# Kernel tuning notes

Measured on AMD Instinct MI355X. Metric: run time of the kernel, lower is better.

## Reference

```python
import jax, jax.numpy as jnp
import numpy as np

H, W, D, C = 32, 16, 16, 4
NUM_ITERS = 2
THETA_GAMMA = 3.0   # spatial (position-only) kernel bandwidth
THETA_ALPHA = 8.0   # bilateral position bandwidth
THETA_BETA = 0.5    # bilateral color bandwidth


def _attn(feats, q):
    # Gaussian-kernel attention: softmax_j(-0.5 * ||f_i - f_j||^2) @ q
    # feats: [N, F], q: [N, C] -> [N, C]
    sq = jnp.sum(feats * feats, axis=-1)
    logits = feats @ feats.T - 0.5 * (sq[:, None] + sq[None, :])  # [N, N]
    return jax.nn.softmax(logits, axis=-1) @ q


def setup_inputs() -> dict:
    key = jax.random.key(0)
    k1, k2 = jax.random.split(key)
    unaries = jax.random.normal(k1, (1, H, W, D, C), dtype=jnp.float32)
    rgb = jax.random.normal(k2, (1, H, W, D, 3), dtype=jnp.float32)
    eye = jnp.eye(C, dtype=jnp.float32)
    return {
        "unaries": unaries,
        "rgb": rgb,
        "spatial_ker_weights": eye,          # _diagonal_initializer
        "bilateral_ker_weights": eye,        # _diagonal_initializer
        "compatibility_matrix": -eye,        # _potts_model_initializer
    }


def reference(unaries, rgb, spatial_ker_weights, bilateral_ker_weights, compatibility_matrix):
    N = H * W * D
    # positions start at 1 as in tf.range(1, h+1)
    grids = jnp.meshgrid(jnp.arange(1, H + 1), jnp.arange(1, W + 1), jnp.arange(1, D + 1), indexing='ij')
    pos = jnp.stack(grids, axis=-1).astype(jnp.float32).reshape(N, 3)
    rgb_flat = rgb.reshape(N, 3)
    spatial_feats = pos / THETA_GAMMA                                             # [N, 3]
    bilateral_feats = jnp.concatenate([pos / THETA_ALPHA, rgb_flat / THETA_BETA], axis=-1)  # [N, 6]

    u = unaries.reshape(N, C)
    q = u
    for _ in range(NUM_ITERS):
        sm = jax.nn.softmax(q, axis=-1)                         # [N, C]
        spatial_out = _attn(spatial_feats, sm)                  # [N, C]
        bilateral_out = _attn(bilateral_feats, sm)              # [N, C]
        # message_passing = SK @ spatial + BK @ bilateral (class-space matmul)
        message = spatial_out @ spatial_ker_weights.T + bilateral_out @ bilateral_ker_weights.T
        pairwise = message @ compatibility_matrix.T             # [N, C]
        q = u + pairwise
    return q.reshape(unaries.shape)
```

## Files before the change

### kernel.cpp

```cpp
#include <hip/hip_runtime.h>


#define HH 32
#define WW 16
#define DDD 16
#define NN (HH * WW * DDD)
#define KS 128
#define JC (NN / KS)
#define GB 2048
#define L2E 1.4426950408889634f
#define C18 (L2E / 18.0f)
#define SQL2E 1.2011224087864498f
#define SB (SQL2E / 8.0f)
#define SC (SQL2E / 0.5f)

#if __has_builtin(__builtin_amdgcn_exp2f)
#define EXP2(x) __builtin_amdgcn_exp2f(x)
#else
#define EXP2(x) exp2f(x)
#endif

__global__ __launch_bounds__(256, 8) void fused_bilat_conv(
    const float* __restrict__ qin,
    const float* __restrict__ rgb,
    float* __restrict__ part,
    float* __restrict__ tmp)
{
    __shared__ float lds[2048];
    int tid = threadIdx.x;

    if (blockIdx.x < GB) {
        int ib = blockIdx.x >> 7;
        int kc = blockIdx.x & (KS - 1);
        int i0 = ib * 512 + tid;
        int i1 = i0 + 256;
        int j0 = kc * JC;

        float fw = (float)(((tid >> 4) & 15) + 1) * SB;
        float fd = (float)((tid & 15) + 1) * SB;
        int hb = ib * 2;
        float fh = (float)(hb + 1) * SB;
        float c00 = rgb[3 * i0 + 0] * SC;
        float c01 = rgb[3 * i0 + 1] * SC;
        float c02 = rgb[3 * i0 + 2] * SC;
        float c10 = rgb[3 * i1 + 0] * SC;
        float c11 = rgb[3 * i1 + 1] * SC;
        float c12 = rgb[3 * i1 + 2] * SC;
        float fh1 = fh + SB;
        float nn0 = -0.5f * (fh * fh + fw * fw + fd * fd +
                             c00 * c00 + c01 * c01 + c02 * c02);
        float nn1 = -0.5f * (fh1 * fh1 + fw * fw + fd * fd +
                             c10 * c10 + c11 * c11 + c12 * c12);
        float dn = nn1 - nn0;
        float dc0 = c10 - c00, dc1 = c11 - c01, dc2 = c12 - c02;

        float (*recs)[12] = (float(*)[12])lds;
        if (tid < JC) {
            int j = j0 + tid;
            int jh = j >> 8, jr = j & 255;
            float gh = (float)(jh + 1) * SB;
            float gw = (float)((jr >> 4) + 1) * SB;
            float gd = (float)((jr & 15) + 1) * SB;
            float b0 = rgb[3 * j + 0] * SC;
            float b1 = rgb[3 * j + 1] * SC;
            float b2 = rgb[3 * j + 2] * SC;
            float nj = -0.5f * (gh * gh + gw * gw + gd * gd +
                                b0 * b0 + b1 * b1 + b2 * b2);
            float4 q = *((const float4*)(qin + 4 * j));
            float m = fmaxf(fmaxf(q.x, q.y), fmaxf(q.z, q.w));
            float e0 = EXP2((q.x - m) * L2E), e1 = EXP2((q.y - m) * L2E);
            float e2 = EXP2((q.z - m) * L2E), e3 = EXP2((q.w - m) * L2E);
            float rs = 1.0f / (e0 + e1 + e2 + e3);
            *((float4*)&recs[tid][0]) = make_float4(gh, gw, gd, b0);
            *((float4*)&recs[tid][4]) = make_float4(b1, b2, nj, 0.0f);
            *((float4*)&recs[tid][8]) = make_float4(e0 * rs, e1 * rs, e2 * rs, e3 * rs);
        }
        __syncthreads();

        float a0 = 0, a1 = 0, a2 = 0, a3 = 0;
        float b0a = 0, b1a = 0, b2a = 0, b3a = 0;

        #pragma unroll 4
        for (int jj = 0; jj < JC; ++jj) {
            const float4 r0 = *((const float4*)&recs[jj][0]);
            const float4 r1 = *((const float4*)&recs[jj][4]);
            const float4 s  = *((const float4*)&recs[jj][8]);
            float g0 = nn0 + r1.z;
            g0 = fmaf(fh,  r0.x, g0);
            g0 = fmaf(fw,  r0.y, g0);
            g0 = fmaf(fd,  r0.z, g0);
            g0 = fmaf(c00, r0.w, g0);
            g0 = fmaf(c01, r1.x, g0);
            g0 = fmaf(c02, r1.y, g0);
            float g1 = g0 + dn;
            g1 = fmaf(SB,  r0.x, g1);
            g1 = fmaf(dc0, r0.w, g1);
            g1 = fmaf(dc1, r1.x, g1);
            g1 = fmaf(dc2, r1.y, g1);
            float w0 = EXP2(g0);
            float w1 = EXP2(g1);
            a0  = fmaf(w0, s.x, a0);  a1  = fmaf(w0, s.y, a1);
            a2  = fmaf(w0, s.z, a2);  a3  = fmaf(w0, s.w, a3);
            b0a = fmaf(w1, s.x, b0a); b1a = fmaf(w1, s.y, b1a);
            b2a = fmaf(w1, s.z, b2a); b3a = fmaf(w1, s.w, b3a);
        }

        float* p = part + (size_t)kc * (NN * 4);
        *((float4*)(p + (size_t)i0 * 4)) = make_float4(a0, a1, a2, a3);
        *((float4*)(p + (size_t)i1 * 4)) = make_float4(b0a, b1a, b2a, b3a);
    } else {
        int h = blockIdx.x - GB;
        int s = tid;
        int i = h * 256 + s;

        float4 q = *((const float4*)(qin + 4 * i));
        float m = fmaxf(fmaxf(q.x, q.y), fmaxf(q.z, q.w));
        float e0 = EXP2((q.x - m) * L2E), e1 = EXP2((q.y - m) * L2E);
        float e2 = EXP2((q.z - m) * L2E), e3 = EXP2((q.w - m) * L2E);
        float rs = 1.0f / (e0 + e1 + e2 + e3);

        float* A = lds;
        float* B = lds + 1024;
        *((float4*)(A + 4 * s)) = make_float4(e0 * rs, e1 * rs, e2 * rs, e3 * rs);
        __syncthreads();

        int w = s >> 4, d = s & 15;
        float t0 = 0, t1 = 0, t2 = 0, t3 = 0;
        #pragma unroll
        for (int dp = 0; dp < DDD; ++dp) {
            float dd = (float)(d - dp);
            float k = EXP2(-dd * dd * C18);
            const float4 v = *((const float4*)(A + 4 * (w * 16 + dp)));
            t0 = fmaf(k, v.x, t0); t1 = fmaf(k, v.y, t1);
            t2 = fmaf(k, v.z, t2); t3 = fmaf(k, v.w, t3);
        }
        *((float4*)(B + 4 * s)) = make_float4(t0, t1, t2, t3);
        __syncthreads();

        float u0 = 0, u1 = 0, u2 = 0, u3 = 0;
        #pragma unroll
        for (int wp = 0; wp < WW; ++wp) {
            float dw = (float)(w - wp);
            float k = EXP2(-dw * dw * C18);
            const float4 v = *((const float4*)(B + 4 * (wp * 16 + d)));
            u0 = fmaf(k, v.x, u0); u1 = fmaf(k, v.y, u1);
            u2 = fmaf(k, v.z, u2); u3 = fmaf(k, v.w, u3);
        }
        *((float4*)(tmp + 4 * i)) = make_float4(u0, u1, u2, u3);
    }
}

__global__ __launch_bounds__(256) void reduce_finish(
    const float* __restrict__ part,
    const float* __restrict__ tmp,
    const float* __restrict__ u,
    const float* __restrict__ sk, const float* __restrict__ bk,
    const float* __restrict__ cm,
    float* __restrict__ qout)
{
    int tid = threadIdx.x;
    int q = tid >> 6;
    int lane = tid & 63;
    int idx = blockIdx.x * 64 + lane;

    float bl = 0.0f;
    #pragma unroll
    for (int k = 0; k < KS / 4; ++k)
        bl += part[(size_t)(q * (KS / 4) + k) * (NN * 4) + idx];

    int i = idx >> 2;
    int h = i >> 8;
    int scid = idx & 1023;
    float sp = 0.0f;
    #pragma unroll
    for (int k = 0; k < 8; ++k) {
        int hp = q * 8 + k;
        float dh = (float)(h - hp);
        float kk = EXP2(-dh * dh * C18);
        sp = fmaf(kk, tmp[hp * 1024 + scid], sp);
    }

    __shared__ float Lb[4][64];
    __shared__ float Ls[4][64];
    Lb[q][lane] = bl;
    Ls[q][lane] = sp;
    __syncthreads();

    if (tid < 16) {
        float b4[4], s4[4];
        #pragma unroll
        for (int c = 0; c < 4; ++c) {
            int l = tid * 4 + c;
            b4[c] = Lb[0][l] + Lb[1][l] + Lb[2][l] + Lb[3][l];
            s4[c] = Ls[0][l] + Ls[1][l] + Ls[2][l] + Ls[3][l];
        }
        float rb = 1.0f / (b4[0] + b4[1] + b4[2] + b4[3]);
        float rs = 1.0f / (s4[0] + s4[1] + s4[2] + s4[3]);
        float bo[4], so[4];
        #pragma unroll
        for (int c = 0; c < 4; ++c) { bo[c] = b4[c] * rb; so[c] = s4[c] * rs; }
        float msg[4];
        #pragma unroll
        for (int c = 0; c < 4; ++c) {
            float m = 0.0f;
            #pragma unroll
            for (int d = 0; d < 4; ++d)
                m += sk[c * 4 + d] * so[d] + bk[c * 4 + d] * bo[d];
            msg[c] = m;
        }
        int ig = blockIdx.x * 16 + tid;
        #pragma unroll
        for (int c = 0; c < 4; ++c) {
            float pw = 0.0f;
            #pragma unroll
            for (int d = 0; d < 4; ++d) pw += cm[c * 4 + d] * msg[d];
            qout[4 * ig + c] = u[4 * ig + c] + pw;
        }
    }
}

extern "C" void kernel_launch(void* const* d_in, const int* in_sizes, int n_in,
                              void* d_out, int out_size, void* d_ws, size_t ws_size,
                              hipStream_t stream)
{
    const float* u   = (const float*)d_in[0];
    const float* rgb = (const float*)d_in[1];
    const float* sk  = (const float*)d_in[2];
    const float* bk  = (const float*)d_in[3];
    const float* cm  = (const float*)d_in[4];
    float* out = (float*)d_out;

    float* part = (float*)d_ws;
    float* tmpP = part + (size_t)KS * NN * 4;
    float* qbuf = tmpP + (size_t)NN * 4;

    dim3 blk(256);
    dim3 gF(GB + HH);
    dim3 gR(NN * 4 / 64);

    fused_bilat_conv<<<gF, blk, 0, stream>>>(u, rgb, part, tmpP);
    reduce_finish<<<gR, blk, 0, stream>>>(part, tmpP, u, sk, bk, cm, qbuf);
    fused_bilat_conv<<<gF, blk, 0, stream>>>(qbuf, rgb, part, tmpP);
    reduce_finish<<<gR, blk, 0, stream>>>(part, tmpP, u, sk, bk, cm, out);
}
```

Measured before the change: 62.36 us.

## Precompute bilateral features and softmax once, reuse across iterations

Adds a prep kernel that computes per-voxel bilateral features (scaled position, color, norm term) and the initial softmax into workspace. The softmax for the next iteration is now produced inside reduce_finish. The main kernel loads features and probabilities from global memory instead of recomputing them per block. The conv blocks are moved to the front of the grid so they get scheduled first. This removes redundant exp and feature arithmetic that was repeated across 128 blocks per j-chunk, at the cost of an extra launch and more global traffic.

Measured after the change: 68.36 us. 1.1x slower.

```diff
diff --git a/kernel.cpp b/kernel.cpp
--- a/kernel.cpp
+++ b/kernel.cpp
@@ -7,6 +7,7 @@
 #define NN (HH * WW * DDD)
 #define KS 128
 #define JC (NN / KS)
+#define CONVB 32
 #define GB 2048
 #define L2E 1.4426950408889634f
 #define C18 (L2E / 18.0f)
@@ -20,108 +21,104 @@
 #define EXP2(x) exp2f(x)
 #endif
 
-__global__ __launch_bounds__(256, 8) void fused_bilat_conv(
-    const float* __restrict__ qin,
-    const float* __restrict__ rgb,
+__global__ __launch_bounds__(256) void prep(
+    const float* __restrict__ u, const float* __restrict__ rgb,
+    float* __restrict__ feats, float* __restrict__ sm0)
+{
+    int i = blockIdx.x * 256 + threadIdx.x;
+    int h = i >> 8, r = i & 255, w = r >> 4, d = r & 15;
+    float fh = (float)(h + 1) * SB;
+    float fw = (float)(w + 1) * SB;
+    float fd = (float)(d + 1) * SB;
+    float c0 = rgb[3 * i + 0] * SC;
+    float c1 = rgb[3 * i + 1] * SC;
+    float c2 = rgb[3 * i + 2] * SC;
+    float nn = -0.5f * (fh * fh + fw * fw + fd * fd + c0 * c0 + c1 * c1 + c2 * c2);
+    ((float4*)feats)[2 * i + 0] = make_float4(fh, fw, fd, c0);
+    ((float4*)feats)[2 * i + 1] = make_float4(c1, c2, nn, 0.0f);
+
+    float4 q = ((const float4*)u)[i];
+    float m = fmaxf(fmaxf(q.x, q.y), fmaxf(q.z, q.w));
+    float e0 = EXP2((q.x - m) * L2E), e1 = EXP2((q.y - m) * L2E);
+    float e2 = EXP2((q.z - m) * L2E), e3 = EXP2((q.w - m) * L2E);
+    float rs = 1.0f / (e0 + e1 + e2 + e3);
+    ((float4*)sm0)[i] = make_float4(e0 * rs, e1 * rs, e2 * rs, e3 * rs);
+}
+
+__global__ __launch_bounds__(256, 8) void fused(
+    const float* __restrict__ sm,
+    const float* __restrict__ feats,
     float* __restrict__ part,
     float* __restrict__ tmp)
 {
     __shared__ float lds[2048];
     int tid = threadIdx.x;
 
-    if (blockIdx.x < GB) {
-        int ib = blockIdx.x >> 7;
-        int kc = blockIdx.x & (KS - 1);
+    if (blockIdx.x >= CONVB) {
+        int b = blockIdx.x - CONVB;
+        int ib = b >> 7;
+        int kc = b & (KS - 1);
         int i0 = ib * 512 + tid;
         int i1 = i0 + 256;
         int j0 = kc * JC;
 
-        float fw = (float)(((tid >> 4) & 15) + 1) * SB;
-        float fd = (float)((tid & 15) + 1) * SB;
-        int hb = ib * 2;
-        float fh = (float)(hb + 1) * SB;
-        float c00 = rgb[3 * i0 + 0] * SC;
-        float c01 = rgb[3 * i0 + 1] * SC;
-        float c02 = rgb[3 * i0 + 2] * SC;
-        float c10 = rgb[3 * i1 + 0] * SC;
-        float c11 = rgb[3 * i1 + 1] * SC;
-        float c12 = rgb[3 * i1 + 2] * SC;
-        float fh1 = fh + SB;
-        float nn0 = -0.5f * (fh * fh + fw * fw + fd * fd +
-                             c00 * c00 + c01 * c01 + c02 * c02);
-        float nn1 = -0.5f * (fh1 * fh1 + fw * fw + fd * fd +
-                             c10 * c10 + c11 * c11 + c12 * c12);
-        float dn = nn1 - nn0;
-        float dc0 = c10 - c00, dc1 = c11 - c01, dc2 = c12 - c02;
-
-        float (*recs)[12] = (float(*)[12])lds;
-        if (tid < JC) {
-            int j = j0 + tid;
-            int jh = j >> 8, jr = j & 255;
-            float gh = (float)(jh + 1) * SB;
-            float gw = (float)((jr >> 4) + 1) * SB;
-            float gd = (float)((jr & 15) + 1) * SB;
-            float b0 = rgb[3 * j + 0] * SC;
-            float b1 = rgb[3 * j + 1] * SC;
-            float b2 = rgb[3 * j + 2] * SC;
-            float nj = -0.5f * (gh * gh + gw * gw + gd * gd +
-                                b0 * b0 + b1 * b1 + b2 * b2);
-            float4 q = *((const float4*)(qin + 4 * j));
-            float m = fmaxf(fmaxf(q.x, q.y), fmaxf(q.z, q.w));
-            float e0 = EXP2((q.x - m) * L2E), e1 = EXP2((q.y - m) * L2E);
-            float e2 = EXP2((q.z - m) * L2E), e3 = EXP2((q.w - m) * L2E);
-            float rs = 1.0f / (e0 + e1 + e2 + e3);
-            *((float4*)&recs[tid][0]) = make_float4(gh, gw, gd, b0);
-            *((float4*)&recs[tid][4]) = make_float4(b1, b2, nj, 0.0f);
-            *((float4*)&recs[tid][8]) = make_float4(e0 * rs, e1 * rs, e2 * rs, e3 * rs);
-        }
+        const float4* f4 = (const float4*)feats;
+        const float4* s4 = (const float4*)sm;
+
+        float4* lrec = (float4*)lds;
+        if (tid < 128) {
+            float4 v = f4[2 * j0 + tid];
+            lrec[(tid >> 1) * 3 + (tid & 1)] = v;
+        } else if (tid < 192) {
+            int jj = tid - 128;
+            lrec[jj * 3 + 2] = s4[j0 + jj];
+        }
+
+        float4 A0 = f4[2 * i0], A1 = f4[2 * i0 + 1];
+        float4 B0 = f4[2 * i1], B1 = f4[2 * i1 + 1];
+        float dfh = B0.x - A0.x;
+        float dc0 = B0.w - A0.w, dc1 = B1.x - A1.x, dc2 = B1.y - A1.y;
+        float dn  = B1.z - A1.z;
         __syncthreads();
 
         float a0 = 0, a1 = 0, a2 = 0, a3 = 0;
-        float b0a = 0, b1a = 0, b2a = 0, b3a = 0;
+        float b0 = 0, b1 = 0, b2 = 0, b3 = 0;
 
         #pragma unroll 4
         for (int jj = 0; jj < JC; ++jj) {
-            const float4 r0 = *((const float4*)&recs[jj][0]);
-            const float4 r1 = *((const float4*)&recs[jj][4]);
-            const float4 s  = *((const float4*)&recs[jj][8]);
-            float g0 = nn0 + r1.z;
-            g0 = fmaf(fh,  r0.x, g0);
-            g0 = fmaf(fw,  r0.y, g0);
-            g0 = fmaf(fd,  r0.z, g0);
-            g0 = fmaf(c00, r0.w, g0);
-            g0 = fmaf(c01, r1.x, g0);
-            g0 = fmaf(c02, r1.y, g0);
-            float g1 = g0 + dn;
-            g1 = fmaf(SB,  r0.x, g1);
+            float4 r0 = lrec[jj * 3 + 0];
+            float4 r1 = lrec[jj * 3 + 1];
+            float4 s  = lrec[jj * 3 + 2];
+            float g0 = A1.z + r1.z;
+            g0 = fmaf(A0.x, r0.x, g0);
+            g0 = fmaf(A0.y, r0.y, g0);
+            g0 = fmaf(A0.z, r0.z, g0);
+            g0 = fmaf(A0.w, r0.w, g0);
+            g0 = fmaf(A1.x, r1.x, g0);
+            g0 = fmaf(A1.y, r1.y, g0);
+            float g1 = fmaf(dfh, r0.x, g0 + dn);
             g1 = fmaf(dc0, r0.w, g1);
             g1 = fmaf(dc1, r1.x, g1);
             g1 = fmaf(dc2, r1.y, g1);
             float w0 = EXP2(g0);
             float w1 = EXP2(g1);
-            a0  = fmaf(w0, s.x, a0);  a1  = fmaf(w0, s.y, a1);
-            a2  = fmaf(w0, s.z, a2);  a3  = fmaf(w0, s.w, a3);
-            b0a = fmaf(w1, s.x, b0a); b1a = fmaf(w1, s.y, b1a);
-            b2a = fmaf(w1, s.z, b2a); b3a = fmaf(w1, s.w, b3a);
-        }
-
-        float* p = part + (size_t)kc * (NN * 4);
-        *((float4*)(p + (size_t)i0 * 4)) = make_float4(a0, a1, a2, a3);
-        *((float4*)(p + (size_t)i1 * 4)) = make_float4(b0a, b1a, b2a, b3a);
+            a0 = fmaf(w0, s.x, a0); a1 = fmaf(w0, s.y, a1);
+            a2 = fmaf(w0, s.z, a2); a3 = fmaf(w0, s.w, a3);
+            b0 = fmaf(w1, s.x, b0); b1 = fmaf(w1, s.y, b1);
+            b2 = fmaf(w1, s.z, b2); b3 = fmaf(w1, s.w, b3);
+        }
+
+        float4* p = (float4*)(part + (size_t)kc * (NN * 4));
+        p[i0] = make_float4(a0, a1, a2, a3);
+        p[i1] = make_float4(b0, b1, b2, b3);
     } else {
-        int h = blockIdx.x - GB;
+        int h = blockIdx.x;
         int s = tid;
         int i = h * 256 + s;
 
-        float4 q = *((const float4*)(qin + 4 * i));
-        float m = fmaxf(fmaxf(q.x, q.y), fmaxf(q.z, q.w));
-        float e0 = EXP2((q.x - m) * L2E), e1 = EXP2((q.y - m) * L2E);
-        float e2 = EXP2((q.z - m) * L2E), e3 = EXP2((q.w - m) * L2E);
-        float rs = 1.0f / (e0 + e1 + e2 + e3);
-
         float* A = lds;
         float* B = lds + 1024;
-        *((float4*)(A + 4 * s)) = make_float4(e0 * rs, e1 * rs, e2 * rs, e3 * rs);
+        *((float4*)(A + 4 * s)) = ((const float4*)sm)[i];
         __syncthreads();
 
         int w = s >> 4, d = s & 15;
@@ -156,7 +153,8 @@
     const float* __restrict__ u,
     const float* __restrict__ sk, const float* __restrict__ bk,
     const float* __restrict__ cm,
-    float* __restrict__ qout)
+    float* __restrict__ qout,
+    float* __restrict__ smout)
 {
     int tid = threadIdx.x;
     int q = tid >> 6;
@@ -209,13 +207,21 @@
             msg[c] = m;
         }
         int ig = blockIdx.x * 16 + tid;
+        float qv[4];
         #pragma unroll
         for (int c = 0; c < 4; ++c) {
             float pw = 0.0f;
             #pragma unroll
             for (int d = 0; d < 4; ++d) pw += cm[c * 4 + d] * msg[d];
-            qout[4 * ig + c] = u[4 * ig + c] + pw;
-        }
+            qv[c] = u[4 * ig + c] + pw;
+        }
+        *((float4*)(qout + 4 * ig)) = make_float4(qv[0], qv[1], qv[2], qv[3]);
+
+        float mm = fmaxf(fmaxf(qv[0], qv[1]), fmaxf(qv[2], qv[3]));
+        float e0 = EXP2((qv[0] - mm) * L2E), e1 = EXP2((qv[1] - mm) * L2E);
+        float e2 = EXP2((qv[2] - mm) * L2E), e3 = EXP2((qv[3] - mm) * L2E);
+        float er = 1.0f / (e0 + e1 + e2 + e3);
+        *((float4*)(smout + 4 * ig)) = make_float4(e0 * er, e1 * er, e2 * er, e3 * er);
     }
 }
 
@@ -230,16 +236,22 @@
     const float* cm  = (const float*)d_in[4];
     float* out = (float*)d_out;
 
-    float* part = (float*)d_ws;
-    float* tmpP = part + (size_t)KS * NN * 4;
-    float* qbuf = tmpP + (size_t)NN * 4;
+    float* part   = (float*)d_ws;
+    float* feats  = part  + (size_t)KS * NN * 4;
+    float* tmpP   = feats + (size_t)NN * 8;
+    float* smA    = tmpP  + (size_t)NN * 4;
+    float* smB    = smA   + (size_t)NN * 4;
+    float* qbuf   = smB   + (size_t)NN * 4;
+    float* smDead = qbuf  + (size_t)NN * 4;
 
     dim3 blk(256);
-    dim3 gF(GB + HH);
+    dim3 gP(NN / 256);
+    dim3 gF(CONVB + GB);
     dim3 gR(NN * 4 / 64);
 
-    fused_bilat_conv<<<gF, blk, 0, stream>>>(u, rgb, part, tmpP);
-    reduce_finish<<<gR, blk, 0, stream>>>(part, tmpP, u, sk, bk, cm, qbuf);
-    fused_bilat_conv<<<gF, blk, 0, stream>>>(qbuf, rgb, part, tmpP);
-    reduce_finish<<<gR, blk, 0, stream>>>(part, tmpP, u, sk, bk, cm, out);
-}
+    prep<<<gP, blk, 0, stream>>>(u, rgb, feats, smA);
+    fused<<<gF, blk, 0, stream>>>(smA, feats, part, tmpP);
+    reduce_finish<<<gR, blk, 0, stream>>>(part, tmpP, u, sk, bk, cm, qbuf, smB);
+    fused<<<gF, blk, 0, stream>>>(smB, feats, part, tmpP);
+    reduce_finish<<<gR, blk, 0, stream>>>(part, tmpP, u, sk, bk, cm, out, smDead);
+}
```

## Fuse each CRF iteration into one kernel with atomic accumulation and bf16 softmax

Applied to the files above, without the earlier changes.

Each mean-field iteration now runs as one kernel instead of a split-K bilateral pass followed by a reduction kernel. Bilateral blocks own 16 query points and loop over all keys in LDS chunks. Within a block, lanes reduce with shuffles and then apply the folded compatibility-times-kernel matrix, while spatial blocks handle the separable conv including the H dimension. Both paths write into a zeroed output through atomicAdd, which removes the large partials buffer and the second launch. In exchange the grid has far fewer blocks, each running a long serial loop, and the softmax probabilities are stored as bf16, which reduces precision.

New measurement: 95.88 us. 53.8% more time.

```diff
diff --git a/kernel.cpp b/kernel.cpp
--- a/kernel.cpp
+++ b/kernel.cpp
@@ -5,9 +5,10 @@
 #define WW 16
 #define DDD 16
 #define NN (HH * WW * DDD)
-#define KS 128
-#define JC (NN / KS)
-#define GB 2048
+#define SPB 32
+#define BILB 512
+#define CHK 512
+#define NCHK (NN / CHK)
 #define L2E 1.4426950408889634f
 #define C18 (L2E / 18.0f)
 #define SQL2E 1.2011224087864498f
@@ -20,111 +21,166 @@
 #define EXP2(x) exp2f(x)
 #endif
 
-__global__ __launch_bounds__(256, 8) void fused_bilat_conv(
-    const float* __restrict__ qin,
+__device__ __forceinline__ float bfLO(unsigned int u) {
+    return __uint_as_float(u << 16);
+}
+__device__ __forceinline__ float bfHI(unsigned int u) {
+    return __uint_as_float(u & 0xFFFF0000u);
+}
+__device__ __forceinline__ unsigned int cvtpk(float lo, float hi) {
+    unsigned int r;
+    asm("v_cvt_pk_bf16_f32 %0, %1, %2" : "=v"(r) : "v"(lo), "v"(hi));
+    return r;
+}
+
+__global__ __launch_bounds__(256) void iter(
+    const float* __restrict__ qcur,
     const float* __restrict__ rgb,
-    float* __restrict__ part,
-    float* __restrict__ tmp)
+    const float* __restrict__ uin,
+    const float* __restrict__ sk, const float* __restrict__ bk,
+    const float* __restrict__ cm,
+    float* __restrict__ qnext)
 {
-    __shared__ float lds[2048];
+    __shared__ float lds[4608];
     int tid = threadIdx.x;
 
-    if (blockIdx.x < GB) {
-        int ib = blockIdx.x >> 7;
-        int kc = blockIdx.x & (KS - 1);
-        int i0 = ib * 512 + tid;
-        int i1 = i0 + 256;
-        int j0 = kc * JC;
-
-        float fw = (float)(((tid >> 4) & 15) + 1) * SB;
-        float fd = (float)((tid & 15) + 1) * SB;
-        int hb = ib * 2;
-        float fh = (float)(hb + 1) * SB;
-        float c00 = rgb[3 * i0 + 0] * SC;
-        float c01 = rgb[3 * i0 + 1] * SC;
-        float c02 = rgb[3 * i0 + 2] * SC;
-        float c10 = rgb[3 * i1 + 0] * SC;
-        float c11 = rgb[3 * i1 + 1] * SC;
-        float c12 = rgb[3 * i1 + 2] * SC;
-        float fh1 = fh + SB;
-        float nn0 = -0.5f * (fh * fh + fw * fw + fd * fd +
-                             c00 * c00 + c01 * c01 + c02 * c02);
-        float nn1 = -0.5f * (fh1 * fh1 + fw * fw + fd * fd +
-                             c10 * c10 + c11 * c11 + c12 * c12);
-        float dn = nn1 - nn0;
-        float dc0 = c10 - c00, dc1 = c11 - c01, dc2 = c12 - c02;
-
-        float (*recs)[12] = (float(*)[12])lds;
-        if (tid < JC) {
-            int j = j0 + tid;
-            int jh = j >> 8, jr = j & 255;
-            float gh = (float)(jh + 1) * SB;
-            float gw = (float)((jr >> 4) + 1) * SB;
-            float gd = (float)((jr & 15) + 1) * SB;
-            float b0 = rgb[3 * j + 0] * SC;
-            float b1 = rgb[3 * j + 1] * SC;
-            float b2 = rgb[3 * j + 2] * SC;
-            float nj = -0.5f * (gh * gh + gw * gw + gd * gd +
-                                b0 * b0 + b1 * b1 + b2 * b2);
-            float4 q = *((const float4*)(qin + 4 * j));
+    if (blockIdx.x >= SPB) {
+        int b = blockIdx.x - SPB;
+        int h = b >> 4, w = b & 15;
+        int ibase = b << 4;
+        int slot = tid >> 5, jlane = tid & 31;
+        int i0 = ibase + slot;
+        int i1 = ibase + slot + 8;
+
+        float fh = (float)(h + 1) * SB;
+        float fw = (float)(w + 1) * SB;
+        float fd0 = (float)(slot + 1) * SB;
+        float fd1 = (float)(slot + 9) * SB;
+        float c00 = rgb[3 * i0] * SC, c01 = rgb[3 * i0 + 1] * SC, c02 = rgb[3 * i0 + 2] * SC;
+        float c10 = rgb[3 * i1] * SC, c11 = rgb[3 * i1 + 1] * SC, c12 = rgb[3 * i1 + 2] * SC;
+        float hw2 = fh * fh + fw * fw;
+        float nn0 = -0.5f * (hw2 + fd0 * fd0 + c00 * c00 + c01 * c01 + c02 * c02);
+        float nn1 = -0.5f * (hw2 + fd1 * fd1 + c10 * c10 + c11 * c11 + c12 * c12);
+
+        float2* gHW = (float2*)lds;
+        float2* gDN = (float2*)(lds + 1024);
+        float2* C01 = (float2*)(lds + 2048);
+        float*  C2a = lds + 3072;
+        uint2*  SMa = (uint2*)(lds + 3584);
+
+        float a0 = 0, a1 = 0, a2 = 0, a3 = 0;
+        float b0 = 0, b1 = 0, b2 = 0, b3 = 0;
+
+        for (int c = 0; c < NCHK; ++c) {
+            __syncthreads();
+            #pragma unroll
+            for (int tt = 0; tt < 2; ++tt) {
+                int t = tid + tt * 256;
+                int j = c * CHK + t;
+                int jh = j >> 8, jr = j & 255, jw = jr >> 4, jd = jr & 15;
+                float gh = (float)(jh + 1) * SB;
+                float gw = (float)(jw + 1) * SB;
+                float gd = (float)(jd + 1) * SB;
+                float e0c = rgb[3 * j] * SC, e1c = rgb[3 * j + 1] * SC, e2c = rgb[3 * j + 2] * SC;
+                float nj = -0.5f * (gh * gh + gw * gw + gd * gd +
+                                    e0c * e0c + e1c * e1c + e2c * e2c);
+                float4 q = ((const float4*)qcur)[j];
+                float m = fmaxf(fmaxf(q.x, q.y), fmaxf(q.z, q.w));
+                float s0 = EXP2((q.x - m) * L2E), s1 = EXP2((q.y - m) * L2E);
+                float s2 = EXP2((q.z - m) * L2E), s3 = EXP2((q.w - m) * L2E);
+                float rs = 1.0f / (s0 + s1 + s2 + s3);
+                gHW[t] = make_float2(gh, gw);
+                gDN[t] = make_float2(gd, nj);
+                C01[t] = make_float2(e0c, e1c);
+                C2a[t] = e2c;
+                SMa[t] = make_uint2(cvtpk(s0 * rs, s1 * rs), cvtpk(s2 * rs, s3 * rs));
+            }
+            __syncthreads();
+
+            #pragma unroll 4
+            for (int k = 0; k < CHK / 32; ++k) {
+                int jl = k * 32 + jlane;
+                float2 gg = gHW[jl];
+                float2 dn = gDN[jl];
+                float2 cc = C01[jl];
+                float c2v = C2a[jl];
+                uint2 sp = SMa[jl];
+                float s0 = bfLO(sp.x), s1 = bfHI(sp.x);
+                float s2 = bfLO(sp.y), s3 = bfHI(sp.y);
+                float bse = fmaf(fh, gg.x, fmaf(fw, gg.y, dn.y));
+                float g0 = fmaf(fd0, dn.x, bse + nn0);
+                g0 = fmaf(c00, cc.x, g0);
+                g0 = fmaf(c01, cc.y, g0);
+                g0 = fmaf(c02, c2v, g0);
+                float g1 = fmaf(fd1, dn.x, bse + nn1);
+                g1 = fmaf(c10, cc.x, g1);
+                g1 = fmaf(c11, cc.y, g1);
+                g1 = fmaf(c12, c2v, g1);
+                float w0 = EXP2(g0);
+                float w1 = EXP2(g1);
+                a0 = fmaf(w0, s0, a0); a1 = fmaf(w0, s1, a1);
+                a2 = fmaf(w0, s2, a2); a3 = fmaf(w0, s3, a3);
+                b0 = fmaf(w1, s0, b0); b1 = fmaf(w1, s1, b1);
+                b2 = fmaf(w1, s2, b2); b3 = fmaf(w1, s3, b3);
+            }
+        }
+
+        #pragma unroll
+        for (int m = 16; m >= 1; m >>= 1) {
+            a0 += __shfl_xor(a0, m); a1 += __shfl_xor(a1, m);
+            a2 += __shfl_xor(a2, m); a3 += __shfl_xor(a3, m);
+            b0 += __shfl_xor(b0, m); b1 += __shfl_xor(b1, m);
+            b2 += __shfl_xor(b2, m); b3 += __shfl_xor(b3, m);
+        }
+
+        if (jlane == 0) {
+            float Mb[4][4];
+            #pragma unroll
+            for (int cR = 0; cR < 4; ++cR)
+                #pragma unroll
+                for (int e = 0; e < 4; ++e) {
+                    float acc = 0.0f;
+                    #pragma unroll
+                    for (int d = 0; d < 4; ++d)
+                        acc += cm[cR * 4 + d] * bk[d * 4 + e];
+                    Mb[cR][e] = acc;
+                }
+            float ra = 1.0f / (a0 + a1 + a2 + a3);
+            float na[4] = { a0 * ra, a1 * ra, a2 * ra, a3 * ra };
+            float rb = 1.0f / (b0 + b1 + b2 + b3);
+            float nb[4] = { b0 * rb, b1 * rb, b2 * rb, b3 * rb };
+            #pragma unroll
+            for (int cR = 0; cR < 4; ++cR) {
+                float va = Mb[cR][0] * na[0] + Mb[cR][1] * na[1] +
+                           Mb[cR][2] * na[2] + Mb[cR][3] * na[3];
+                float vb = Mb[cR][0] * nb[0] + Mb[cR][1] * nb[1] +
+                           Mb[cR][2] * nb[2] + Mb[cR][3] * nb[3];
+                atomicAdd(&qnext[4 * i0 + cR], va);
+                atomicAdd(&qnext[4 * i1 + cR], vb);
+            }
+        }
+    } else {
+        int h = blockIdx.x;
+        int s = tid;
+        int w = s >> 4, d = s & 15;
+
+        float h0 = 0, h1 = 0, h2 = 0, h3 = 0;
+        for (int hp = 0; hp < HH; ++hp) {
+            float4 q = ((const float4*)qcur)[hp * 256 + s];
             float m = fmaxf(fmaxf(q.x, q.y), fmaxf(q.z, q.w));
-            float e0 = EXP2((q.x - m) * L2E), e1 = EXP2((q.y - m) * L2E);
-            float e2 = EXP2((q.z - m) * L2E), e3 = EXP2((q.w - m) * L2E);
-            float rs = 1.0f / (e0 + e1 + e2 + e3);
-            *((float4*)&recs[tid][0]) = make_float4(gh, gw, gd, b0);
-            *((float4*)&recs[tid][4]) = make_float4(b1, b2, nj, 0.0f);
-            *((float4*)&recs[tid][8]) = make_float4(e0 * rs, e1 * rs, e2 * rs, e3 * rs);
-        }
-        __syncthreads();
-
-        float a0 = 0, a1 = 0, a2 = 0, a3 = 0;
-        float b0a = 0, b1a = 0, b2a = 0, b3a = 0;
-
-        #pragma unroll 4
-        for (int jj = 0; jj < JC; ++jj) {
-            const float4 r0 = *((const float4*)&recs[jj][0]);
-            const float4 r1 = *((const float4*)&recs[jj][4]);
-            const float4 s  = *((const float4*)&recs[jj][8]);
-            float g0 = nn0 + r1.z;
-            g0 = fmaf(fh,  r0.x, g0);
-            g0 = fmaf(fw,  r0.y, g0);
-            g0 = fmaf(fd,  r0.z, g0);
-            g0 = fmaf(c00, r0.w, g0);
-            g0 = fmaf(c01, r1.x, g0);
-            g0 = fmaf(c02, r1.y, g0);
-            float g1 = g0 + dn;
-            g1 = fmaf(SB,  r0.x, g1);
-            g1 = fmaf(dc0, r0.w, g1);
-            g1 = fmaf(dc1, r1.x, g1);
-            g1 = fmaf(dc2, r1.y, g1);
-            float w0 = EXP2(g0);
-            float w1 = EXP2(g1);
-            a0  = fmaf(w0, s.x, a0);  a1  = fmaf(w0, s.y, a1);
-            a2  = fmaf(w0, s.z, a2);  a3  = fmaf(w0, s.w, a3);
-            b0a = fmaf(w1, s.x, b0a); b1a = fmaf(w1, s.y, b1a);
-            b2a = fmaf(w1, s.z, b2a); b3a = fmaf(w1, s.w, b3a);
-        }
-
-        float* p = part + (size_t)kc * (NN * 4);
-        *((float4*)(p + (size_t)i0 * 4)) = make_float4(a0, a1, a2, a3);
-        *((float4*)(p + (size_t)i1 * 4)) = make_float4(b0a, b1a, b2a, b3a);
-    } else {
-        int h = blockIdx.x - GB;
-        int s = tid;
-        int i = h * 256 + s;
-
-        float4 q = *((const float4*)(qin + 4 * i));
-        float m = fmaxf(fmaxf(q.x, q.y), fmaxf(q.z, q.w));
-        float e0 = EXP2((q.x - m) * L2E), e1 = EXP2((q.y - m) * L2E);
-        float e2 = EXP2((q.z - m) * L2E), e3 = EXP2((q.w - m) * L2E);
-        float rs = 1.0f / (e0 + e1 + e2 + e3);
-
+            float s0 = EXP2((q.x - m) * L2E), s1 = EXP2((q.y - m) * L2E);
+            float s2 = EXP2((q.z - m) * L2E), s3 = EXP2((q.w - m) * L2E);
+            float rs = 1.0f / (s0 + s1 + s2 + s3);
+            float dh = (float)(h - hp);
+            float kh = EXP2(-dh * dh * C18) * rs;
+            h0 = fmaf(kh, s0, h0); h1 = fmaf(kh, s1, h1);
+            h2 = fmaf(kh, s2, h2); h3 = fmaf(kh, s3, h3);
+        }
         float* A = lds;
         float* B = lds + 1024;
-        *((float4*)(A + 4 * s)) = make_float4(e0 * rs, e1 * rs, e2 * rs, e3 * rs);
+        *((float4*)(A + 4 * s)) = make_float4(h0, h1, h2, h3);
         __syncthreads();
 
-        int w = s >> 4, d = s & 15;
         float t0 = 0, t1 = 0, t2 = 0, t3 = 0;
         #pragma unroll
         for (int dp = 0; dp < DDD; ++dp) {
@@ -146,75 +202,26 @@
             u0 = fmaf(k, v.x, u0); u1 = fmaf(k, v.y, u1);
             u2 = fmaf(k, v.z, u2); u3 = fmaf(k, v.w, u3);
         }
-        *((float4*)(tmp + 4 * i)) = make_float4(u0, u1, u2, u3);
-    }
-}
-
-__global__ __launch_bounds__(256) void reduce_finish(
-    const float* __restrict__ part,
-    const float* __restrict__ tmp,
-    const float* __restrict__ u,
-    const float* __restrict__ sk, const float* __restrict__ bk,
-    const float* __restrict__ cm,
-    float* __restrict__ qout)
-{
-    int tid = threadIdx.x;
-    int q = tid >> 6;
-    int lane = tid & 63;
-    int idx = blockIdx.x * 64 + lane;
-
-    float bl = 0.0f;
-    #pragma unroll
-    for (int k = 0; k < KS / 4; ++k)
-        bl += part[(size_t)(q * (KS / 4) + k) * (NN * 4) + idx];
-
-    int i = idx >> 2;
-    int h = i >> 8;
-    int scid = idx & 1023;
-    float sp = 0.0f;
-    #pragma unroll
-    for (int k = 0; k < 8; ++k) {
-        int hp = q * 8 + k;
-        float dh = (float)(h - hp);
-        float kk = EXP2(-dh * dh * C18);
-        sp = fmaf(kk, tmp[hp * 1024 + scid], sp);
-    }
-
-    __shared__ float Lb[4][64];
-    __shared__ float Ls[4][64];
-    Lb[q][lane] = bl;
-    Ls[q][lane] = sp;
-    __syncthreads();
-
-    if (tid < 16) {
-        float b4[4], s4[4];
-        #pragma unroll
-        for (int c = 0; c < 4; ++c) {
-            int l = tid * 4 + c;
-            b4[c] = Lb[0][l] + Lb[1][l] + Lb[2][l] + Lb[3][l];
-            s4[c] = Ls[0][l] + Ls[1][l] + Ls[2][l] + Ls[3][l];
-        }
-        float rb = 1.0f / (b4[0] + b4[1] + b4[2] + b4[3]);
-        float rs = 1.0f / (s4[0] + s4[1] + s4[2] + s4[3]);
-        float bo[4], so[4];
-        #pragma unroll
-        for (int c = 0; c < 4; ++c) { bo[c] = b4[c] * rb; so[c] = s4[c] * rs; }
-        float msg[4];
-        #pragma unroll
-        for (int c = 0; c < 4; ++c) {
-            float m = 0.0f;
-            #pragma unroll
-            for (int d = 0; d < 4; ++d)
-                m += sk[c * 4 + d] * so[d] + bk[c * 4 + d] * bo[d];
-            msg[c] = m;
-        }
-        int ig = blockIdx.x * 16 + tid;
-        #pragma unroll
-        for (int c = 0; c < 4; ++c) {
-            float pw = 0.0f;
-            #pragma unroll
-            for (int d = 0; d < 4; ++d) pw += cm[c * 4 + d] * msg[d];
-            qout[4 * ig + c] = u[4 * ig + c] + pw;
+
+        float Ms[4][4];
+        #pragma unroll
+        for (int cR = 0; cR < 4; ++cR)
+            #pragma unroll
+            for (int e = 0; e < 4; ++e) {
+                float acc = 0.0f;
+                #pragma unroll
+                for (int dd2 = 0; dd2 < 4; ++dd2)
+                    acc += cm[cR * 4 + dd2] * sk[dd2 * 4 + e];
+                Ms[cR][e] = acc;
+            }
+        float rs = 1.0f / (u0 + u1 + u2 + u3);
+        float ns[4] = { u0 * rs, u1 * rs, u2 * rs, u3 * rs };
+        int ig = h * 256 + s;
+        #pragma unroll
+        for (int cR = 0; cR < 4; ++cR) {
+            float v = Ms[cR][0] * ns[0] + Ms[cR][1] * ns[1] +
+                      Ms[cR][2] * ns[2] + Ms[cR][3] * ns[3];
+            atomicAdd(&qnext[4 * ig + cR], uin[4 * ig + cR] + v);
         }
     }
 }
@@ -230,16 +237,14 @@
     const float* cm  = (const float*)d_in[4];
     float* out = (float*)d_out;
 
-    float* part = (float*)d_ws;
-    float* tmpP = part + (size_t)KS * NN * 4;
-    float* qbuf = tmpP + (size_t)NN * 4;
+    float* q1 = (float*)d_ws;
+
+    hipMemsetAsync(q1, 0, (size_t)NN * 4 * sizeof(float), stream);
+    hipMemsetAsync(out, 0, (size_t)NN * 4 * sizeof(float), stream);
 
     dim3 blk(256);
-    dim3 gF(GB + HH);
-    dim3 gR(NN * 4 / 64);
-
-    fused_bilat_conv<<<gF, blk, 0, stream>>>(u, rgb, part, tmpP);
-    reduce_finish<<<gR, blk, 0, stream>>>(part, tmpP, u, sk, bk, cm, qbuf);
-    fused_bilat_conv<<<gF, blk, 0, stream>>>(qbuf, rgb, part, tmpP);
-    reduce_finish<<<gR, blk, 0, stream>>>(part, tmpP, u, sk, bk, cm, out);
-}
+    dim3 grd(SPB + BILB);
+
+    iter<<<grd, blk, 0, stream>>>(u, rgb, u, sk, bk, cm, q1);
+    iter<<<grd, blk, 0, stream>>>(q1, rgb, u, sk, bk, cm, out);
+}
```
